# Performance work log

Hardware: AMD Instinct MI355X
Metric: run time of the kernel (lower is better)

The kernel has to match this reference:

```python
import jax, jax.numpy as jnp
import numpy as np

R_MAX = 5.0
AVG_NEIGH = 16.0
NUM_RADIAL = 8
F = 64            # channels per irrep (num_features)
S = 10            # num_species
LDIM = 16         # (max_ell+1)^2 for max_ell=3
L_SLICES = [(0, 1), (1, 4), (4, 9), (9, 16)]  # lm ranges for l=0..3
N_NODES = 10000
N_EDGES = 160000
HID_R = 64        # radial MLP hidden
HID_READ = 32     # readout MLP hidden


def sph_harm(v):
    # real spherical-harmonic polynomials up to l=3 (component convention fixed by this reference)
    x, y, z = v[:, 0], v[:, 1], v[:, 2]
    r2 = x * x + y * y + z * z
    return jnp.stack([
        jnp.ones_like(x),
        x, y, z,
        x * y, y * z, 3.0 * z * z - r2, x * z, x * x - y * y,
        y * (3.0 * x * x - y * y), x * y * z, y * (5.0 * z * z - r2),
        z * (5.0 * z * z - 3.0 * r2), x * (5.0 * z * z - r2),
        z * (x * x - y * y), x * (x * x - 3.0 * y * y),
    ], axis=-1)  # [E,16]


def radial_embedding(r):
    # Bessel basis with polynomial envelope (RadialEmbeddingBlock)
    u = r / R_MAX
    k = jnp.arange(1, NUM_RADIAL + 1, dtype=r.dtype)
    env = jnp.where(u < 1.0, (1.0 - u) ** 2 * (1.0 + 2.0 * u), 0.0)
    return jnp.sin(jnp.pi * k[None, :] * u[:, None]) / (u[:, None] + 1e-6) * env[:, None]


def species_linear(feats, W):
    # species-indexed e3nn Linear: per-l channel mixing. feats [N,F,16], W [N,4,F,F]
    outs = []
    for l, (a, b) in enumerate(L_SLICES):
        outs.append(jnp.einsum('nfm,nfg->ngm', feats[:, :, a:b], W[:, l]))
    return jnp.concatenate(outs, axis=-1)


def interaction(feats, Y, Remb, w1, w2, senders, receivers, n_nodes):
    # InteractionBlock: radial MLP -> tensor-product messages -> scatter-sum
    E = Y.shape[0]
    R = (jax.nn.silu(Remb @ w1) @ w2).reshape(E, F, 4, 2)  # per-l, per-path radial weights
    fs = feats[senders]            # [E,F,16] gather (irregular access)
    s0 = fs[:, :, 0:1]             # sender scalar channel
    parts = []
    for l, (a, b) in enumerate(L_SLICES):
        # path A: 0e (x) l -> l ;  path B: l (x) 0e -> l
        m_l = R[:, :, l, 0:1] * s0 * Y[:, None, a:b] + R[:, :, l, 1:2] * fs[:, :, a:b]
        parts.append(m_l)
    m = jnp.concatenate(parts, axis=-1)  # [E,F,16]
    agg = jax.ops.segment_sum(m, receivers, num_segments=n_nodes)
    return agg / jnp.sqrt(jnp.asarray(AVG_NEIGH, m.dtype))


def setup_inputs() -> dict:
    key = jax.random.key(0)
    ks = jax.random.split(key, 16)
    inp = {
        'vectors': jax.random.normal(ks[0], (N_EDGES, 3), jnp.float32) * 1.5,
        'node_specie': jax.random.randint(ks[1], (N_NODES,), 0, S, jnp.int32),
        'senders': jax.random.randint(ks[2], (N_EDGES,), 0, N_NODES, jnp.int32),
        'receivers': jax.random.randint(ks[3], (N_EDGES,), 0, N_NODES, jnp.int32),
        'w_embed': jax.random.normal(ks[4], (S, F), jnp.float32),
        'w_r1': jax.random.normal(ks[5], (2, NUM_RADIAL, HID_R), jnp.float32) / np.sqrt(NUM_RADIAL),
        'w_r2': jax.random.normal(ks[6], (2, HID_R, F * 4 * 2), jnp.float32) / np.sqrt(HID_R),
        'w_skip': jax.random.normal(ks[7], (2, S, 4, F, F), jnp.float32) / np.sqrt(F),
        'w_poly': jax.random.normal(ks[8], (2, 3, S, F), jnp.float32) * 0.1,
        'w_read0': jax.random.normal(ks[9], (F, 1), jnp.float32) / np.sqrt(F),
        'w_mlp1': jax.random.normal(ks[10], (F, HID_READ), jnp.float32) / np.sqrt(F),
        'w_mlp2': jax.random.normal(ks[11], (HID_READ, 1), jnp.float32) / np.sqrt(HID_READ),
    }
    return inp


def reference(vectors, node_specie, senders, receivers,
              w_embed, w_r1, w_r2, w_skip, w_poly,
              w_read0, w_mlp1, w_mlp2):
    N = node_specie.shape[0]
    senders = senders.astype(jnp.int32)
    receivers = receivers.astype(jnp.int32)
    r = jnp.sqrt(jnp.sum(vectors ** 2, axis=-1) + 1e-12)
    Y = sph_harm(vectors / r[:, None])
    Remb = radial_embedding(r)
    # node embedding -> scalar (l=0) channel only
    feats = jnp.zeros((N, F, LDIM), vectors.dtype).at[:, :, 0].set(w_embed[node_specie])
    outs = []
    for i in range(2):
        Wn = w_skip[i][node_specie]  # [N,4,F,F] species-indexed weights
        if i == 0:
            agg = interaction(feats, Y, Remb, w_r1[i], w_r2[i], senders, receivers, N)
            h = species_linear(agg, Wn)   # skip_tp_first
            sc = None
        else:
            sc = species_linear(feats, Wn)  # skip connection
            h = interaction(feats, Y, Remb, w_r1[i], w_r2[i], senders, receivers, N)
        # EquivariantProductBasisBlock (correlation=3): degree-3 invariant polynomial gate
        c = w_poly[i][:, node_specie]       # [3,N,F]
        s = h[:, :, 0]
        scale = c[0] + c[1] * s + c[2] * s * s
        feats = h * scale[:, :, None]
        if sc is not None:
            feats = feats + sc
        if i == 0:
            outs.append(feats[:, :, 0] @ w_read0)                       # LinearReadoutBlock
        else:
            outs.append(jax.nn.silu(feats[:, :, 0] @ w_mlp1) @ w_mlp2)  # NonLinearReadoutBlock
    return jnp.stack(outs, axis=1)  # [N, num_interactions, 1]
```

## Files before the change

### kernel.cpp

```cpp
#include <hip/hip_runtime.h>
#include <math.h>

#define F 64
#define LDIM 16
#define NRAD 8
#define HID_R 64
#define HID_READ 32
#define NSPEC 10

typedef __attribute__((ext_vector_type(8))) short short8v;
typedef __attribute__((ext_vector_type(4))) float f32x4;

__device__ __forceinline__ int l_of_m(int m) {
    return (m == 0) ? 0 : (m < 4) ? 1 : (m < 9) ? 2 : 3;
}
__device__ __forceinline__ float silu(float x) { return x / (1.0f + __expf(-x)); }
__device__ __forceinline__ unsigned short bf16bits(float x) {
    unsigned int u = __float_as_uint(x);
    u += 0x7fffu + ((u >> 16) & 1u);
    return (unsigned short)(u >> 16);
}
__device__ __forceinline__ float bf16tof(unsigned short b) {
    return __uint_as_float(((unsigned int)b) << 16);
}
__device__ __forceinline__ float lanebcast(float v, int l) {
    return __uint_as_float(__builtin_amdgcn_readlane(__float_as_uint(v), l));
}

__device__ __forceinline__ void geo_core(const float* __restrict__ vectors, int e,
                                         float* Ye_out, float* remb_out) {
    float vx = vectors[e * 3 + 0];
    float vy = vectors[e * 3 + 1];
    float vz = vectors[e * 3 + 2];
    float r = sqrtf(vx * vx + vy * vy + vz * vz + 1e-12f);
    float x = vx / r, y = vy / r, z = vz / r;
    float r2 = x * x + y * y + z * z;
    Ye_out[0]  = 1.0f;  Ye_out[1] = x;  Ye_out[2] = y;  Ye_out[3] = z;
    Ye_out[4]  = x * y; Ye_out[5] = y * z; Ye_out[6] = 3.0f * z * z - r2; Ye_out[7] = x * z;
    Ye_out[8]  = x * x - y * y;
    Ye_out[9]  = y * (3.0f * x * x - y * y);
    Ye_out[10] = x * y * z;
    Ye_out[11] = y * (5.0f * z * z - r2);
    Ye_out[12] = z * (5.0f * z * z - 3.0f * r2);
    Ye_out[13] = x * (5.0f * z * z - r2);
    Ye_out[14] = z * (x * x - y * y);
    Ye_out[15] = x * (x * x - 3.0f * y * y);
    float u = r / 5.0f;
    float env = (u < 1.0f) ? (1.0f - u) * (1.0f - u) * (1.0f + 2.0f * u) : 0.0f;
    float inv = env / (u + 1e-6f);
    const float PI = 3.14159265358979323846f;
#pragma unroll
    for (int k = 1; k <= NRAD; k++) remb_out[k - 1] = sinf(PI * (float)k * u) * inv;
}

__device__ __forceinline__ void hid_write(const float* remb, const float* w1,
                                          unsigned short* __restrict__ Hb, int e) {
    float h[HID_R];
#pragma unroll
    for (int j = 0; j < HID_R; j++) {
        float a = 0.0f;
#pragma unroll
        for (int k = 0; k < NRAD; k++) a += remb[k] * w1[k * HID_R + j];
        h[j] = silu(a);
    }
    unsigned int* dst = (unsigned int*)(Hb + (size_t)e * HID_R);
#pragma unroll
    for (int w = 0; w < 32; w++) {
        unsigned int lo = bf16bits(h[2 * w]);
        unsigned int hi = bf16bits(h[2 * w + 1]);
        dst[w] = lo | (hi << 16);
    }
}

__global__ void k1_kernel(const float* __restrict__ vectors,
                          const float* __restrict__ w_r1,
                          const float* __restrict__ w_r2,
                          const int* __restrict__ receivers,
                          float* __restrict__ Y,
                          unsigned short* __restrict__ Hb,
                          int* __restrict__ cnt,
                          unsigned short* __restrict__ w2f,
                          int E, int ngeo) {
    const int bid = blockIdx.x;
    if (bid >= ngeo) {
        const int layer = bid - ngeo;
        const float* src = w_r2 + (size_t)layer * HID_R * 512;
        unsigned short* dst = w2f + (size_t)layer * 32768;
        for (int idx = threadIdx.x; idx < 32768; idx += 256) {
            int j    = idx & 7;
            int lane = (idx >> 3) & 63;
            int ks   = (idx >> 9) & 1;
            int ct   = idx >> 10;
            int k    = ks * 32 + (lane >> 4) * 8 + j;
            int col  = ct * 16 + (lane & 15);
            dst[idx] = bf16bits(src[k * 512 + col]);
        }
        return;
    }
    const int e = bid * 256 + threadIdx.x;
    if (e >= E) return;
    atomicAdd(&cnt[receivers[e]], 1);
    float ye[16], remb[NRAD];
    geo_core(vectors, e, ye, remb);
    float4* Yd = (float4*)(Y + (size_t)e * 16);
    Yd[0] = make_float4(ye[0], ye[1], ye[2], ye[3]);
    Yd[1] = make_float4(ye[4], ye[5], ye[6], ye[7]);
    Yd[2] = make_float4(ye[8], ye[9], ye[10], ye[11]);
    Yd[3] = make_float4(ye[12], ye[13], ye[14], ye[15]);
    hid_write(remb, w_r1, Hb, e);
}

__global__ void geo_kernel(const float* __restrict__ vectors,
                           float* __restrict__ Y, float* __restrict__ Remb, int E) {
    int e = blockIdx.x * 256 + threadIdx.x;
    if (e >= E) return;
    float ye[16], remb[NRAD];
    geo_core(vectors, e, ye, remb);
#pragma unroll
    for (int m = 0; m < 16; m++) Y[(size_t)e * 16 + m] = ye[m];
#pragma unroll
    for (int k = 0; k < NRAD; k++) Remb[(size_t)e * NRAD + k] = remb[k];
}

__global__ void scan_kernel(const int* __restrict__ cnt, int* __restrict__ offs, int N) {
    __shared__ int buf[1024];
    __shared__ int carry;
    int t = threadIdx.x;
    if (t == 0) carry = 0;
    __syncthreads();
    for (int base = 0; base < N; base += 1024) {
        int v = (base + t < N) ? cnt[base + t] : 0;
        buf[t] = v;
        __syncthreads();
#pragma unroll
        for (int off = 1; off < 1024; off <<= 1) {
            int x = (t >= off) ? buf[t - off] : 0;
            __syncthreads();
            buf[t] += x;
            __syncthreads();
        }
        if (base + t < N) offs[base + t] = carry + buf[t] - v;
        __syncthreads();
        if (t == 0) carry += buf[1023];
        __syncthreads();
    }
    if (t == 0) offs[N] = carry;
}

__global__ void scatter_kernel(const int* __restrict__ receivers,
                               const int* __restrict__ senders,
                               const int* __restrict__ offs, int* __restrict__ cur,
                               int* __restrict__ eidx, int* __restrict__ snd_csr,
                               int* __restrict__ rcv_csr, int E) {
    int e = blockIdx.x * 256 + threadIdx.x;
    if (e >= E) return;
    int r = receivers[e];
    int pos = atomicAdd(&cur[r], 1);
    int t = offs[r] + pos;
    eidx[t] = e;
    snd_csr[t] = senders[e];
    rcv_csr[t] = r;
}

__global__ void init_feats_kernel(const float* __restrict__ w_embed,
                                  const int* __restrict__ specie,
                                  float* __restrict__ feats_t, int N) {
    int n = blockIdx.x;
    int sp = specie[n];
    for (int i = threadIdx.x; i < F * LDIM; i += 256) {
        int m = i >> 6;
        int f = i & 63;
        feats_t[(size_t)n * (F * LDIM) + i] = (m == 0) ? w_embed[sp * F + f] : 0.0f;
    }
}

template <bool L0>
__global__ __launch_bounds__(256, 4)
void fused_edge_kernel(const unsigned short* __restrict__ Hb,
                       const unsigned short* __restrict__ w2fl,
                       const float* __restrict__ Y,
                       const unsigned short* __restrict__ featsB,
                       const float* __restrict__ w_embed,
                       const int* __restrict__ specie,
                       const int* __restrict__ offs,
                       const int* __restrict__ eidx,
                       const int* __restrict__ snd_csr,
                       const int* __restrict__ rcv_csr,
                       float* __restrict__ agg, int N) {
    __shared__ float R_lds[16 * 532];
    __shared__ float ysL[16][16];
    __shared__ int   ssL[16];
    __shared__ int   rsL[16];
    const int tid = threadIdx.x;
    const int wave = tid >> 6, lane = tid & 63;
    const int lo = lane & 15, hi = lane >> 4;
    const int n0 = blockIdx.x * 2;
    const int segS = offs[n0], segE = offs[n0 + 2];
    const int mbase = wave * 4;

    int cur = -1;
    float acc[4] = {0.f, 0.f, 0.f, 0.f};

    for (int base = segS; base < segE; base += 16) {
        const int bend = (base + 16 < segE) ? base + 16 : segE;
        const int tcnt = bend - base;
        {
            const int t = tid >> 4, m = tid & 15;
            const int pos = base + t;
            const int cp = (pos < segE) ? pos : (segE - 1);
            ysL[t][m] = Y[(size_t)eidx[cp] * 16 + m];
            if (tid < 16) {
                const int p2 = base + tid;
                const int c2 = (p2 < segE) ? p2 : (segE - 1);
                const int s = snd_csr[c2];
                ssL[tid] = L0 ? specie[s] : s;
                rsL[tid] = rcv_csr[c2];
            }
        }
        {
            const int pos = base + lo;
            const int cp = (pos < segE) ? pos : (segE - 1);
            const int eid = eidx[cp];
            const unsigned short* hrow = Hb + (size_t)eid * 64;
            const short8v a0 = *(const short8v*)(hrow + hi * 8);
            const short8v a1 = *(const short8v*)(hrow + 32 + hi * 8);
            f32x4 c16[8];
#pragma unroll
            for (int i = 0; i < 8; i++) c16[i] = (f32x4)(0.f);
#pragma unroll
            for (int tt = 0; tt < 8; tt++) {
                const int ct = wave * 8 + tt;
                const short8v b0 = *(const short8v*)(w2fl + ct * 1024 + lane * 8);
                const short8v b1 = *(const short8v*)(w2fl + ct * 1024 + 512 + lane * 8);
                c16[tt] = __builtin_amdgcn_mfma_f32_16x16x32_bf16(a0, b0, c16[tt], 0, 0, 0);
                c16[tt] = __builtin_amdgcn_mfma_f32_16x16x32_bf16(a1, b1, c16[tt], 0, 0, 0);
            }
            const int lc = lo & 7;
#pragma unroll
            for (int tt = 0; tt < 8; tt++) {
                const int ct = wave * 8 + tt;
                const int f = ct * 2 + (lo >> 3);
#pragma unroll
                for (int r = 0; r < 4; r++) {
                    const int el = hi * 4 + r;
                    R_lds[el * 532 + lc * 66 + f] = c16[tt][r];
                }
            }
        }
        __syncthreads();
        {
            float ps0, pf[4] = {0.f, 0.f, 0.f, 0.f};
            if (L0) {
                ps0 = w_embed[ssL[0] * 64 + lane];
            } else {
                const unsigned short* f_ = featsB + (size_t)ssL[0] * 1024;
                ps0 = bf16tof(f_[lane]);
#pragma unroll
                for (int j = 0; j < 4; j++) pf[j] = bf16tof(f_[(mbase + j) * 64 + lane]);
            }
            for (int k = 0; k < tcnt; k++) {
                float ns0 = 0.f, nf[4] = {0.f, 0.f, 0.f, 0.f};
                const int kn = (k + 1 < tcnt) ? k + 1 : k;
                if (L0) {
                    ns0 = w_embed[ssL[kn] * 64 + lane];
                } else {
                    const unsigned short* f_ = featsB + (size_t)ssL[kn] * 1024;
                    ns0 = bf16tof(f_[lane]);
#pragma unroll
                    for (int j = 0; j < 4; j++) nf[j] = bf16tof(f_[(mbase + j) * 64 + lane]);
                }
                const int node = rsL[k];
                if (node != cur) {
                    if (cur >= 0) {
#pragma unroll
                        for (int j = 0; j < 4; j++)
                            agg[(size_t)cur * 1024 + (mbase + j) * 64 + lane] = acc[j] * 0.25f;
                    }
#pragma unroll
                    for (int j = 0; j < 4; j++) acc[j] = 0.f;
                    cur = node;
                }
                const float* Rt = R_lds + k * 532;
#pragma unroll
                for (int j = 0; j < 4; j++) {
                    const int m = mbase + j;
                    const int l = l_of_m(m);
                    const float r0 = Rt[(2 * l) * 66 + lane];
                    const float r1 = Rt[(2 * l + 1) * 66 + lane];
                    const float ym = ysL[k][m];
                    const float fsm = L0 ? ((m == 0) ? ps0 : 0.f) : pf[j];
                    acc[j] += r0 * ps0 * ym + r1 * fsm;
                }
                ps0 = ns0;
                if (!L0) {
#pragma unroll
                    for (int j = 0; j < 4; j++) pf[j] = nf[j];
                }
            }
        }
        __syncthreads();
    }
    if (cur >= 0) {
#pragma unroll
        for (int j = 0; j < 4; j++)
            agg[(size_t)cur * 1024 + (mbase + j) * 64 + lane] = acc[j] * 0.25f;
    }
#pragma unroll
    for (int d = 0; d < 2; d++) {
        const int nn = n0 + d;
        if (nn < N && offs[nn] == offs[nn + 1]) {
#pragma unroll
            for (int j = 0; j < 4; j++)
                agg[(size_t)nn * 1024 + (mbase + j) * 64 + lane] = 0.f;
        }
    }
}

__global__ void k2_kernel(const float* __restrict__ agg,
                          const int* __restrict__ specie,
                          const float* __restrict__ w_skip0,
                          const float* __restrict__ w_poly0,
                          const float* __restrict__ w_read0,
                          unsigned short* __restrict__ featsB,
                          float* __restrict__ featsF,
                          int useBF16,
                          float* __restrict__ out, int N,
                          const float* __restrict__ vectors,
                          const float* __restrict__ w1L1,
                          unsigned short* __restrict__ Hb, int E) {
    if (blockIdx.x >= N) {
        const int e = (blockIdx.x - N) * 256 + threadIdx.x;
        if (e >= E) return;
        float ye[16], remb[NRAD];
        geo_core(vectors, e, ye, remb);
        hid_write(remb, w1L1, Hb, e);
        return;
    }
    const int n = blockIdx.x;
    const int g = threadIdx.x & 63;
    const int mb = threadIdx.x >> 6;
    const int sp = specie[n];
    const float* W = w_skip0 + (size_t)sp * 4 * F * F;

    float areg[4];
#pragma unroll
    for (int j = 0; j < 4; j++) areg[j] = agg[(size_t)n * 1024 + (mb * 4 + j) * 64 + g];

    float h[4] = {0.f, 0.f, 0.f, 0.f};
    if (mb == 0) {
        const float* W0 = W;
        const float* W1 = W + 4096;
#pragma unroll
        for (int f = 0; f < 64; f++) {
            const float w0 = W0[f * 64 + g];
            const float w1 = W1[f * 64 + g];
            h[0] += lanebcast(areg[0], f) * w0;
            h[1] += lanebcast(areg[1], f) * w1;
            h[2] += lanebcast(areg[2], f) * w1;
            h[3] += lanebcast(areg[3], f) * w1;
        }
    } else if (mb == 1) {
        const float* W2 = W + 8192;
#pragma unroll
        for (int f = 0; f < 64; f++) {
            const float w2 = W2[f * 64 + g];
            h[0] += lanebcast(areg[0], f) * w2;
            h[1] += lanebcast(areg[1], f) * w2;
            h[2] += lanebcast(areg[2], f) * w2;
            h[3] += lanebcast(areg[3], f) * w2;
        }
    } else if (mb == 2) {
        const float* W2 = W + 8192;
        const float* W3 = W + 12288;
#pragma unroll
        for (int f = 0; f < 64; f++) {
            const float w2 = W2[f * 64 + g];
            const float w3 = W3[f * 64 + g];
            h[0] += lanebcast(areg[0], f) * w2;
            h[1] += lanebcast(areg[1], f) * w3;
            h[2] += lanebcast(areg[2], f) * w3;
            h[3] += lanebcast(areg[3], f) * w3;
        }
    } else {
        const float* W3 = W + 12288;
#pragma unroll
        for (int f = 0; f < 64; f++) {
            const float w3 = W3[f * 64 + g];
            h[0] += lanebcast(areg[0], f) * w3;
            h[1] += lanebcast(areg[1], f) * w3;
            h[2] += lanebcast(areg[2], f) * w3;
            h[3] += lanebcast(areg[3], f) * w3;
        }
    }

    __shared__ float h0L[64];
    if (mb == 0) h0L[g] = h[0];
    __syncthreads();
    const float s = h0L[g];
    const float c0 = w_poly0[(0 * NSPEC + sp) * F + g];
    const float c1 = w_poly0[(1 * NSPEC + sp) * F + g];
    const float c2 = w_poly0[(2 * NSPEC + sp) * F + g];
    const float scale = c0 + c1 * s + c2 * s * s;
    float f0val = 0.0f;
#pragma unroll
    for (int j = 0; j < 4; j++) {
        const int m = mb * 4 + j;
        const float fv = h[j] * scale;
        const size_t idx = (size_t)n * 1024 + m * 64 + g;
        if (useBF16) featsB[idx] = bf16bits(fv);
        else         featsF[idx] = fv;
        if (m == 0) f0val = fv;
    }
    if (mb == 0) {
        float v = f0val * w_read0[g];
#pragma unroll
        for (int off = 32; off > 0; off >>= 1) v += __shfl_down(v, off);
        if (g == 0) out[(size_t)n * 2 + 0] = v;
    }
}

__global__ void node1_kernel(const float* __restrict__ agg,
                             const unsigned short* __restrict__ featsB,
                             const int* __restrict__ specie,
                             const float* __restrict__ w_skip1,
                             const float* __restrict__ w_poly1,
                             const float* __restrict__ w_mlp1,
                             const float* __restrict__ w_mlp2,
                             float* __restrict__ out, int N) {
    const int wave = threadIdx.x >> 6;
    const int lane = threadIdx.x & 63;
    const int n = blockIdx.x * 4 + wave;
    const int sp = specie[n];
    const float* W0 = w_skip1 + (size_t)sp * 4 * F * F;
    const float fv = bf16tof(featsB[(size_t)n * 1024 + lane]);
    float sc0 = 0.0f;
#pragma unroll
    for (int f = 0; f < F; f++) {
        sc0 += lanebcast(fv, f) * W0[f * F + lane];
    }
    const float h0 = agg[(size_t)n * 1024 + lane];
    const float c0 = w_poly1[(0 * NSPEC + sp) * F + lane];
    const float c1 = w_poly1[(1 * NSPEC + sp) * F + lane];
    const float c2 = w_poly1[(2 * NSPEC + sp) * F + lane];
    const float scale = c0 + c1 * h0 + c2 * h0 * h0;
    const float f2 = h0 * scale + sc0;
    float acc = 0.0f;
#pragma unroll
    for (int gg = 0; gg < F; gg++) {
        const float fg = lanebcast(f2, gg);
        if (lane < HID_READ) acc += fg * w_mlp1[gg * HID_READ + lane];
    }
    float o = 0.0f;
    if (lane < HID_READ) o = silu(acc) * w_mlp2[lane];
#pragma unroll
    for (int off = 32; off > 0; off >>= 1) o += __shfl_down(o, off);
    if (lane == 0) out[(size_t)n * 2 + 1] = o;
}

__global__ void node1f_kernel(const float* __restrict__ agg,
                              const float* __restrict__ feats,
                              const int* __restrict__ specie,
                              const float* __restrict__ w_skip1,
                              const float* __restrict__ w_poly1,
                              const float* __restrict__ w_mlp1,
                              const float* __restrict__ w_mlp2,
                              float* __restrict__ out, int N) {
    const int wave = threadIdx.x >> 6;
    const int lane = threadIdx.x & 63;
    const int n = blockIdx.x * 4 + wave;
    const int sp = specie[n];
    const float* W0 = w_skip1 + (size_t)sp * 4 * F * F;
    const float fv = feats[(size_t)n * 1024 + lane];
    float sc0 = 0.0f;
#pragma unroll 8
    for (int f = 0; f < F; f++) {
        const float ff = __shfl(fv, f);
        sc0 += ff * W0[f * F + lane];
    }
    const float h0 = agg[(size_t)n * 1024 + lane];
    const float c0 = w_poly1[(0 * NSPEC + sp) * F + lane];
    const float c1 = w_poly1[(1 * NSPEC + sp) * F + lane];
    const float c2 = w_poly1[(2 * NSPEC + sp) * F + lane];
    const float scale = c0 + c1 * h0 + c2 * h0 * h0;
    const float f2 = h0 * scale + sc0;
    float acc = 0.0f;
#pragma unroll 8
    for (int gg = 0; gg < F; gg++) {
        const float fg = __shfl(f2, gg);
        if (lane < HID_READ) acc += fg * w_mlp1[gg * HID_READ + lane];
    }
    float o = 0.0f;
    if (lane < HID_READ) o = silu(acc) * w_mlp2[lane];
#pragma unroll
    for (int off = 32; off > 0; off >>= 1) o += __shfl_down(o, off);
    if (lane == 0) out[(size_t)n * 2 + 1] = o;
}

__global__ void edge_kernel(const float* __restrict__ Y, const float* __restrict__ Remb,
                            const float* __restrict__ feats_t,
                            const int* __restrict__ senders, const int* __restrict__ receivers,
                            const float* __restrict__ w1, const float* __restrict__ w2,
                            float* __restrict__ agg_t, int E) {
    const int wave = threadIdx.x >> 6;
    const int lane = threadIdx.x & 63;
    const int e = blockIdx.x * 4 + wave;
    __shared__ float hbuf[4][64];
    const float* remb = Remb + (size_t)e * NRAD;
    float acc = 0.0f;
#pragma unroll
    for (int k = 0; k < NRAD; k++) acc += remb[k] * w1[k * F + lane];
    hbuf[wave][lane] = silu(acc);
    __syncthreads();
    float r8[8] = {0.f, 0.f, 0.f, 0.f, 0.f, 0.f, 0.f, 0.f};
    const float* w2base = w2 + lane * 8;
#pragma unroll 8
    for (int j = 0; j < HID_R; j++) {
        float hj = hbuf[wave][j];
        const float4 a = *(const float4*)(w2base + j * 512);
        const float4 b = *(const float4*)(w2base + j * 512 + 4);
        r8[0] += hj * a.x; r8[1] += hj * a.y; r8[2] += hj * a.z; r8[3] += hj * a.w;
        r8[4] += hj * b.x; r8[5] += hj * b.y; r8[6] += hj * b.z; r8[7] += hj * b.w;
    }
    const int snd = senders[e];
    const int rcv = receivers[e];
    const float* fsrc = feats_t + (size_t)snd * (F * LDIM);
    float* adst = agg_t + (size_t)rcv * (F * LDIM);
    const float s0 = fsrc[lane];
    const float* Ye = Y + (size_t)e * 16;
#pragma unroll
    for (int m = 0; m < LDIM; m++) {
        const int l = l_of_m(m);
        const float ym = Ye[m];
        const float fsm = fsrc[m * F + lane];
        const float val = r8[l * 2 + 0] * s0 * ym + r8[l * 2 + 1] * fsm;
        atomicAdd(adst + m * F + lane, val * 0.25f);
    }
}

static inline size_t alignup(size_t x) { return (x + 255) & ~(size_t)255; }

extern "C" void kernel_launch(void* const* d_in, const int* in_sizes, int n_in,
                              void* d_out, int out_size, void* d_ws, size_t ws_size,
                              hipStream_t stream) {
    const float* vectors   = (const float*)d_in[0];
    const int*   specie    = (const int*)d_in[1];
    const int*   senders   = (const int*)d_in[2];
    const int*   receivers = (const int*)d_in[3];
    const float* w_embed   = (const float*)d_in[4];
    const float* w_r1      = (const float*)d_in[5];
    const float* w_r2      = (const float*)d_in[6];
    const float* w_skip    = (const float*)d_in[7];
    const float* w_poly    = (const float*)d_in[8];
    const float* w_read0   = (const float*)d_in[9];
    const float* w_mlp1    = (const float*)d_in[10];
    const float* w_mlp2    = (const float*)d_in[11];
    float* out = (float*)d_out;

    const int E = in_sizes[0] / 3;
    const int N = in_sizes[1];
    const int ngeo = (E + 255) / 256;

    char* base = (char*)d_ws;
    size_t off = 0;
    float* Y      = (float*)(base + off); off += alignup((size_t)E * 16 * sizeof(float));
    unsigned short* featsB = (unsigned short*)(base + off); off += alignup((size_t)N * F * LDIM * sizeof(unsigned short));
    float* agg    = (float*)(base + off); off += alignup((size_t)N * F * LDIM * sizeof(float));
    unsigned short* Hb = (unsigned short*)(base + off); off += alignup((size_t)E * 64 * sizeof(unsigned short));
    int* cnt      = (int*)(base + off);   off += alignup((size_t)N * sizeof(int));
    int* cur      = (int*)(base + off);   off += alignup((size_t)N * sizeof(int));
    int* offs     = (int*)(base + off);   off += alignup((size_t)(N + 1) * sizeof(int));
    int* eidx     = (int*)(base + off);   off += alignup((size_t)E * sizeof(int));
    int* snd_csr  = (int*)(base + off);   off += alignup((size_t)E * sizeof(int));
    int* rcv_csr  = (int*)(base + off);   off += alignup((size_t)E * sizeof(int));
    unsigned short* w2f = (unsigned short*)(base + off); off += alignup((size_t)2 * 32768 * sizeof(unsigned short));
    const size_t need = off;

    const size_t aggBytes = (size_t)N * F * LDIM * sizeof(float);

    if (ws_size >= need) {
        hipMemsetAsync(cnt, 0, (size_t)N * sizeof(int), stream);
        hipMemsetAsync(cur, 0, (size_t)N * sizeof(int), stream);
        k1_kernel<<<ngeo + 2, 256, 0, stream>>>(vectors, w_r1, w_r2, receivers,
                                                Y, Hb, cnt, w2f, E, ngeo);
        scan_kernel<<<1, 1024, 0, stream>>>(cnt, offs, N);
        scatter_kernel<<<ngeo, 256, 0, stream>>>(receivers, senders, offs, cur,
                                                 eidx, snd_csr, rcv_csr, E);
        fused_edge_kernel<true><<<N / 2, 256, 0, stream>>>(
            Hb, w2f, Y, nullptr, w_embed, specie, offs, eidx, snd_csr, rcv_csr, agg, N);
        k2_kernel<<<N + ngeo, 256, 0, stream>>>(agg, specie,
                                                w_skip + (size_t)0 * NSPEC * 4 * F * F,
                                                w_poly + (size_t)0 * 3 * NSPEC * F,
                                                w_read0, featsB, nullptr, 1, out, N,
                                                vectors, w_r1 + NRAD * HID_R, Hb, E);
        fused_edge_kernel<false><<<N / 2, 256, 0, stream>>>(
            Hb, w2f + 32768, Y, featsB, w_embed, specie, offs, eidx, snd_csr, rcv_csr, agg, N);
        node1_kernel<<<N / 4, 256, 0, stream>>>(agg, featsB, specie,
                                                w_skip + (size_t)1 * NSPEC * 4 * F * F,
                                                w_poly + (size_t)1 * 3 * NSPEC * F,
                                                w_mlp1, w_mlp2, out, N);
    } else {
        size_t fo = 0;
        float* Yf    = (float*)(base + fo); fo += alignup((size_t)E * 16 * sizeof(float));
        float* Remb  = (float*)(base + fo); fo += alignup((size_t)E * NRAD * sizeof(float));
        float* featsF= (float*)(base + fo); fo += alignup((size_t)N * F * LDIM * sizeof(float));
        float* aggF  = (float*)(base + fo);

        geo_kernel<<<ngeo, 256, 0, stream>>>(vectors, Yf, Remb, E);
        init_feats_kernel<<<N, 256, 0, stream>>>(w_embed, specie, featsF, N);
        hipMemsetAsync(aggF, 0, aggBytes, stream);
        edge_kernel<<<E / 4, 256, 0, stream>>>(Yf, Remb, featsF, senders, receivers,
                                               w_r1, w_r2, aggF, E);
        k2_kernel<<<N, 256, 0, stream>>>(aggF, specie,
                                         w_skip + (size_t)0 * NSPEC * 4 * F * F,
                                         w_poly + (size_t)0 * 3 * NSPEC * F,
                                         w_read0, nullptr, featsF, 0, out, N,
                                         vectors, w_r1 + NRAD * HID_R, nullptr, 0);
        hipMemsetAsync(aggF, 0, aggBytes, stream);
        edge_kernel<<<E / 4, 256, 0, stream>>>(Yf, Remb, featsF, senders, receivers,
                                               w_r1 + NRAD * HID_R, w_r2 + HID_R * 512,
                                               aggF, E);
        node1f_kernel<<<N / 4, 256, 0, stream>>>(aggF, featsF, specie,
                                                 w_skip + (size_t)1 * NSPEC * 4 * F * F,
                                                 w_poly + (size_t)1 * 3 * NSPEC * F,
                                                 w_mlp1, w_mlp2, out, N);
    }
}
```

Measured before the change: 360.9 us.

## Fuse node-level species linear, gate and readout into edge aggregation kernels

Each fused edge kernel now keeps its per-node accumulators for its two receiver nodes in registers and directly applies the species-indexed linear, polynomial gate and readout, instead of writing agg to global memory and launching k2/node1 kernels. The layer-1 radial hidden activations are computed up front in k1 into a second buffer, removing that work from k2. This drops the agg round trip and two launches, but adds per-block serial matmul work (64x64 per l) that sits at the tail of the edge kernel and may lower occupancy. It also now requires an even node count.

```diff
diff --git a/kernel.cpp b/kernel.cpp
--- a/kernel.cpp
+++ b/kernel.cpp
@@ -77,7 +77,8 @@
                           const float* __restrict__ w_r2,
                           const int* __restrict__ receivers,
                           float* __restrict__ Y,
-                          unsigned short* __restrict__ Hb,
+                          unsigned short* __restrict__ Hb0,
+                          unsigned short* __restrict__ Hb1,
                           int* __restrict__ cnt,
                           unsigned short* __restrict__ w2f,
                           int E, int ngeo) {
@@ -107,7 +108,8 @@
     Yd[1] = make_float4(ye[4], ye[5], ye[6], ye[7]);
     Yd[2] = make_float4(ye[8], ye[9], ye[10], ye[11]);
     Yd[3] = make_float4(ye[12], ye[13], ye[14], ye[15]);
-    hid_write(remb, w_r1, Hb, e);
+    hid_write(remb, w_r1, Hb0, e);
+    hid_write(remb, w_r1 + NRAD * HID_R, Hb1, e);
 }
 
 __global__ void geo_kernel(const float* __restrict__ vectors,
@@ -179,18 +181,26 @@
 void fused_edge_kernel(const unsigned short* __restrict__ Hb,
                        const unsigned short* __restrict__ w2fl,
                        const float* __restrict__ Y,
-                       const unsigned short* __restrict__ featsB,
+                       const unsigned short* __restrict__ featsIn,
                        const float* __restrict__ w_embed,
                        const int* __restrict__ specie,
                        const int* __restrict__ offs,
                        const int* __restrict__ eidx,
                        const int* __restrict__ snd_csr,
                        const int* __restrict__ rcv_csr,
-                       float* __restrict__ agg, int N) {
+                       const float* __restrict__ w_skipL,
+                       const float* __restrict__ w_polyL,
+                       const float* __restrict__ w_read0,
+                       const float* __restrict__ w_mlp1,
+                       const float* __restrict__ w_mlp2,
+                       unsigned short* __restrict__ featsOut,
+                       float* __restrict__ out, int N) {
     __shared__ float R_lds[16 * 532];
     __shared__ float ysL[16][16];
     __shared__ int   ssL[16];
     __shared__ int   rsL[16];
+    __shared__ float h0LA[64];
+    __shared__ float h0LB[64];
     const int tid = threadIdx.x;
     const int wave = tid >> 6, lane = tid & 63;
     const int lo = lane & 15, hi = lane >> 4;
@@ -198,8 +208,8 @@
     const int segS = offs[n0], segE = offs[n0 + 2];
     const int mbase = wave * 4;
 
-    int cur = -1;
-    float acc[4] = {0.f, 0.f, 0.f, 0.f};
+    float accA[4] = {0.f, 0.f, 0.f, 0.f};
+    float accB[4] = {0.f, 0.f, 0.f, 0.f};
 
     for (int base = segS; base < segE; base += 16) {
         const int bend = (base + 16 < segE) ? base + 16 : segE;
@@ -253,7 +263,7 @@
             if (L0) {
                 ps0 = w_embed[ssL[0] * 64 + lane];
             } else {
-                const unsigned short* f_ = featsB + (size_t)ssL[0] * 1024;
+                const unsigned short* f_ = featsIn + (size_t)ssL[0] * 1024;
                 ps0 = bf16tof(f_[lane]);
 #pragma unroll
                 for (int j = 0; j < 4; j++) pf[j] = bf16tof(f_[(mbase + j) * 64 + lane]);
@@ -264,32 +274,35 @@
                 if (L0) {
                     ns0 = w_embed[ssL[kn] * 64 + lane];
                 } else {
-                    const unsigned short* f_ = featsB + (size_t)ssL[kn] * 1024;
+                    const unsigned short* f_ = featsIn + (size_t)ssL[kn] * 1024;
                     ns0 = bf16tof(f_[lane]);
 #pragma unroll
                     for (int j = 0; j < 4; j++) nf[j] = bf16tof(f_[(mbase + j) * 64 + lane]);
                 }
                 const int node = rsL[k];
-                if (node != cur) {
-                    if (cur >= 0) {
-#pragma unroll
-                        for (int j = 0; j < 4; j++)
-                            agg[(size_t)cur * 1024 + (mbase + j) * 64 + lane] = acc[j] * 0.25f;
+                const float* Rt = R_lds + k * 532;
+                if (node == n0) {
+#pragma unroll
+                    for (int j = 0; j < 4; j++) {
+                        const int m = mbase + j;
+                        const int l = l_of_m(m);
+                        const float r0 = Rt[(2 * l) * 66 + lane];
+                        const float r1 = Rt[(2 * l + 1) * 66 + lane];
+                        const float ym = ysL[k][m];
+                        const float fsm = L0 ? ((m == 0) ? ps0 : 0.f) : pf[j];
+                        accA[j] += r0 * ps0 * ym + r1 * fsm;
                     }
-#pragma unroll
-                    for (int j = 0; j < 4; j++) acc[j] = 0.f;
-                    cur = node;
-                }
-                const float* Rt = R_lds + k * 532;
-#pragma unroll
-                for (int j = 0; j < 4; j++) {
-                    const int m = mbase + j;
-                    const int l = l_of_m(m);
-                    const float r0 = Rt[(2 * l) * 66 + lane];
-                    const float r1 = Rt[(2 * l + 1) * 66 + lane];
-                    const float ym = ysL[k][m];
-                    const float fsm = L0 ? ((m == 0) ? ps0 : 0.f) : pf[j];
-                    acc[j] += r0 * ps0 * ym + r1 * fsm;
+                } else {
+#pragma unroll
+                    for (int j = 0; j < 4; j++) {
+                        const int m = mbase + j;
+                        const int l = l_of_m(m);
+                        const float r0 = Rt[(2 * l) * 66 + lane];
+                        const float r1 = Rt[(2 * l + 1) * 66 + lane];
+                        const float ym = ysL[k][m];
+                        const float fsm = L0 ? ((m == 0) ? ps0 : 0.f) : pf[j];
+                        accB[j] += r0 * ps0 * ym + r1 * fsm;
+                    }
                 }
                 ps0 = ns0;
                 if (!L0) {
@@ -300,18 +313,158 @@
         }
         __syncthreads();
     }
-    if (cur >= 0) {
-#pragma unroll
-        for (int j = 0; j < 4; j++)
-            agg[(size_t)cur * 1024 + (mbase + j) * 64 + lane] = acc[j] * 0.25f;
-    }
-#pragma unroll
-    for (int d = 0; d < 2; d++) {
-        const int nn = n0 + d;
-        if (nn < N && offs[nn] == offs[nn + 1]) {
-#pragma unroll
-            for (int j = 0; j < 4; j++)
-                agg[(size_t)nn * 1024 + (mbase + j) * 64 + lane] = 0.f;
+
+    const int nA = n0, nB = n0 + 1;
+    const int spA = specie[nA], spB = specie[nB];
+    const int g = lane;
+
+    if (L0) {
+        float aA[4], aB[4];
+#pragma unroll
+        for (int j = 0; j < 4; j++) { aA[j] = accA[j] * 0.25f; aB[j] = accB[j] * 0.25f; }
+        const float* WA = w_skipL + (size_t)spA * 4 * F * F;
+        const float* WB = w_skipL + (size_t)spB * 4 * F * F;
+        float hA[4] = {0.f, 0.f, 0.f, 0.f};
+        float hB[4] = {0.f, 0.f, 0.f, 0.f};
+        if (wave == 0) {
+            const float *WA0 = WA, *WA1 = WA + 4096, *WB0 = WB, *WB1 = WB + 4096;
+#pragma unroll
+            for (int f = 0; f < 64; f++) {
+                const float wa0 = WA0[f * 64 + g], wa1 = WA1[f * 64 + g];
+                const float wb0 = WB0[f * 64 + g], wb1 = WB1[f * 64 + g];
+                hA[0] += lanebcast(aA[0], f) * wa0;
+                hA[1] += lanebcast(aA[1], f) * wa1;
+                hA[2] += lanebcast(aA[2], f) * wa1;
+                hA[3] += lanebcast(aA[3], f) * wa1;
+                hB[0] += lanebcast(aB[0], f) * wb0;
+                hB[1] += lanebcast(aB[1], f) * wb1;
+                hB[2] += lanebcast(aB[2], f) * wb1;
+                hB[3] += lanebcast(aB[3], f) * wb1;
+            }
+        } else if (wave == 1) {
+            const float *WA2 = WA + 8192, *WB2 = WB + 8192;
+#pragma unroll
+            for (int f = 0; f < 64; f++) {
+                const float wa2 = WA2[f * 64 + g], wb2 = WB2[f * 64 + g];
+                hA[0] += lanebcast(aA[0], f) * wa2;
+                hA[1] += lanebcast(aA[1], f) * wa2;
+                hA[2] += lanebcast(aA[2], f) * wa2;
+                hA[3] += lanebcast(aA[3], f) * wa2;
+                hB[0] += lanebcast(aB[0], f) * wb2;
+                hB[1] += lanebcast(aB[1], f) * wb2;
+                hB[2] += lanebcast(aB[2], f) * wb2;
+                hB[3] += lanebcast(aB[3], f) * wb2;
+            }
+        } else if (wave == 2) {
+            const float *WA2 = WA + 8192, *WA3 = WA + 12288;
+            const float *WB2 = WB + 8192, *WB3 = WB + 12288;
+#pragma unroll
+            for (int f = 0; f < 64; f++) {
+                const float wa2 = WA2[f * 64 + g], wa3 = WA3[f * 64 + g];
+                const float wb2 = WB2[f * 64 + g], wb3 = WB3[f * 64 + g];
+                hA[0] += lanebcast(aA[0], f) * wa2;
+                hA[1] += lanebcast(aA[1], f) * wa3;
+                hA[2] += lanebcast(aA[2], f) * wa3;
+                hA[3] += lanebcast(aA[3], f) * wa3;
+                hB[0] += lanebcast(aB[0], f) * wb2;
+                hB[1] += lanebcast(aB[1], f) * wb3;
+                hB[2] += lanebcast(aB[2], f) * wb3;
+                hB[3] += lanebcast(aB[3], f) * wb3;
+            }
+        } else {
+            const float *WA3 = WA + 12288, *WB3 = WB + 12288;
+#pragma unroll
+            for (int f = 0; f < 64; f++) {
+                const float wa3 = WA3[f * 64 + g], wb3 = WB3[f * 64 + g];
+                hA[0] += lanebcast(aA[0], f) * wa3;
+                hA[1] += lanebcast(aA[1], f) * wa3;
+                hA[2] += lanebcast(aA[2], f) * wa3;
+                hA[3] += lanebcast(aA[3], f) * wa3;
+                hB[0] += lanebcast(aB[0], f) * wb3;
+                hB[1] += lanebcast(aB[1], f) * wb3;
+                hB[2] += lanebcast(aB[2], f) * wb3;
+                hB[3] += lanebcast(aB[3], f) * wb3;
+            }
+        }
+        if (wave == 0) { h0LA[g] = hA[0]; h0LB[g] = hB[0]; }
+        __syncthreads();
+        const float sA = h0LA[g], sB = h0LB[g];
+        const float c0A = w_polyL[(0 * NSPEC + spA) * F + g];
+        const float c1A = w_polyL[(1 * NSPEC + spA) * F + g];
+        const float c2A = w_polyL[(2 * NSPEC + spA) * F + g];
+        const float scaleA = c0A + c1A * sA + c2A * sA * sA;
+        const float c0B = w_polyL[(0 * NSPEC + spB) * F + g];
+        const float c1B = w_polyL[(1 * NSPEC + spB) * F + g];
+        const float c2B = w_polyL[(2 * NSPEC + spB) * F + g];
+        const float scaleB = c0B + c1B * sB + c2B * sB * sB;
+#pragma unroll
+        for (int j = 0; j < 4; j++) {
+            featsOut[(size_t)nA * 1024 + (mbase + j) * 64 + g] = bf16bits(hA[j] * scaleA);
+            featsOut[(size_t)nB * 1024 + (mbase + j) * 64 + g] = bf16bits(hB[j] * scaleB);
+        }
+        if (wave == 0) {
+            float vA = (hA[0] * scaleA) * w_read0[g];
+            float vB = (hB[0] * scaleB) * w_read0[g];
+#pragma unroll
+            for (int off = 32; off > 0; off >>= 1) {
+                vA += __shfl_down(vA, off);
+                vB += __shfl_down(vB, off);
+            }
+            if (g == 0) {
+                out[(size_t)nA * 2 + 0] = vA;
+                out[(size_t)nB * 2 + 0] = vB;
+            }
+        }
+    } else {
+        if (wave == 0) {
+            {
+                const float* W0 = w_skipL + (size_t)spA * 4 * F * F;
+                const float fv = bf16tof(featsIn[(size_t)nA * 1024 + lane]);
+                float sc0 = 0.0f;
+#pragma unroll
+                for (int f = 0; f < F; f++) sc0 += lanebcast(fv, f) * W0[f * F + lane];
+                const float h0 = accA[0] * 0.25f;
+                const float c0 = w_polyL[(0 * NSPEC + spA) * F + lane];
+                const float c1 = w_polyL[(1 * NSPEC + spA) * F + lane];
+                const float c2 = w_polyL[(2 * NSPEC + spA) * F + lane];
+                const float scale = c0 + c1 * h0 + c2 * h0 * h0;
+                const float f2 = h0 * scale + sc0;
+                float mac = 0.0f;
+#pragma unroll
+                for (int gg = 0; gg < F; gg++) {
+                    const float fg = lanebcast(f2, gg);
+                    if (lane < HID_READ) mac += fg * w_mlp1[gg * HID_READ + lane];
+                }
+                float o = 0.0f;
+                if (lane < HID_READ) o = silu(mac) * w_mlp2[lane];
+#pragma unroll
+                for (int off = 32; off > 0; off >>= 1) o += __shfl_down(o, off);
+                if (lane == 0) out[(size_t)nA * 2 + 1] = o;
+            }
+            {
+                const float* W0 = w_skipL + (size_t)spB * 4 * F * F;
+                const float fv = bf16tof(featsIn[(size_t)nB * 1024 + lane]);
+                float sc0 = 0.0f;
+#pragma unroll
+                for (int f = 0; f < F; f++) sc0 += lanebcast(fv, f) * W0[f * F + lane];
+                const float h0 = accB[0] * 0.25f;
+                const float c0 = w_polyL[(0 * NSPEC + spB) * F + lane];
+                const float c1 = w_polyL[(1 * NSPEC + spB) * F + lane];
+                const float c2 = w_polyL[(2 * NSPEC + spB) * F + lane];
+                const float scale = c0 + c1 * h0 + c2 * h0 * h0;
+                const float f2 = h0 * scale + sc0;
+                float mac = 0.0f;
+#pragma unroll
+                for (int gg = 0; gg < F; gg++) {
+                    const float fg = lanebcast(f2, gg);
+                    if (lane < HID_READ) mac += fg * w_mlp1[gg * HID_READ + lane];
+                }
+                float o = 0.0f;
+                if (lane < HID_READ) o = silu(mac) * w_mlp2[lane];
+#pragma unroll
+                for (int off = 32; off > 0; off >>= 1) o += __shfl_down(o, off);
+                if (lane == 0) out[(size_t)nB * 2 + 1] = o;
+            }
         }
     }
 }
@@ -321,21 +474,8 @@
                           const float* __restrict__ w_skip0,
                           const float* __restrict__ w_poly0,
                           const float* __restrict__ w_read0,
-                          unsigned short* __restrict__ featsB,
                           float* __restrict__ featsF,
-                          int useBF16,
-                          float* __restrict__ out, int N,
-                          const float* __restrict__ vectors,
-                          const float* __restrict__ w1L1,
-                          unsigned short* __restrict__ Hb, int E) {
-    if (blockIdx.x >= N) {
-        const int e = (blockIdx.x - N) * 256 + threadIdx.x;
-        if (e >= E) return;
-        float ye[16], remb[NRAD];
-        geo_core(vectors, e, ye, remb);
-        hid_write(remb, w1L1, Hb, e);
-        return;
-    }
+                          float* __restrict__ out, int N) {
     const int n = blockIdx.x;
     const int g = threadIdx.x & 63;
     const int mb = threadIdx.x >> 6;
@@ -406,9 +546,7 @@
     for (int j = 0; j < 4; j++) {
         const int m = mb * 4 + j;
         const float fv = h[j] * scale;
-        const size_t idx = (size_t)n * 1024 + m * 64 + g;
-        if (useBF16) featsB[idx] = bf16bits(fv);
-        else         featsF[idx] = fv;
+        featsF[(size_t)n * 1024 + m * 64 + g] = fv;
         if (m == 0) f0val = fv;
     }
     if (mb == 0) {
@@ -417,44 +555,6 @@
         for (int off = 32; off > 0; off >>= 1) v += __shfl_down(v, off);
         if (g == 0) out[(size_t)n * 2 + 0] = v;
     }
-}
-
-__global__ void node1_kernel(const float* __restrict__ agg,
-                             const unsigned short* __restrict__ featsB,
-                             const int* __restrict__ specie,
-                             const float* __restrict__ w_skip1,
-                             const float* __restrict__ w_poly1,
-                             const float* __restrict__ w_mlp1,
-                             const float* __restrict__ w_mlp2,
-                             float* __restrict__ out, int N) {
-    const int wave = threadIdx.x >> 6;
-    const int lane = threadIdx.x & 63;
-    const int n = blockIdx.x * 4 + wave;
-    const int sp = specie[n];
-    const float* W0 = w_skip1 + (size_t)sp * 4 * F * F;
-    const float fv = bf16tof(featsB[(size_t)n * 1024 + lane]);
-    float sc0 = 0.0f;
-#pragma unroll
-    for (int f = 0; f < F; f++) {
-        sc0 += lanebcast(fv, f) * W0[f * F + lane];
-    }
-    const float h0 = agg[(size_t)n * 1024 + lane];
-    const float c0 = w_poly1[(0 * NSPEC + sp) * F + lane];
-    const float c1 = w_poly1[(1 * NSPEC + sp) * F + lane];
-    const float c2 = w_poly1[(2 * NSPEC + sp) * F + lane];
-    const float scale = c0 + c1 * h0 + c2 * h0 * h0;
-    const float f2 = h0 * scale + sc0;
-    float acc = 0.0f;
-#pragma unroll
-    for (int gg = 0; gg < F; gg++) {
-        const float fg = lanebcast(f2, gg);
-        if (lane < HID_READ) acc += fg * w_mlp1[gg * HID_READ + lane];
-    }
-    float o = 0.0f;
-    if (lane < HID_READ) o = silu(acc) * w_mlp2[lane];
-#pragma unroll
-    for (int off = 32; off > 0; off >>= 1) o += __shfl_down(o, off);
-    if (lane == 0) out[(size_t)n * 2 + 1] = o;
 }
 
 __global__ void node1f_kernel(const float* __restrict__ agg,
@@ -564,8 +664,8 @@
     size_t off = 0;
     float* Y      = (float*)(base + off); off += alignup((size_t)E * 16 * sizeof(float));
     unsigned short* featsB = (unsigned short*)(base + off); off += alignup((size_t)N * F * LDIM * sizeof(unsigned short));
-    float* agg    = (float*)(base + off); off += alignup((size_t)N * F * LDIM * sizeof(float));
-    unsigned short* Hb = (unsigned short*)(base + off); off += alignup((size_t)E * 64 * sizeof(unsigned short));
+    unsigned short* Hb0 = (unsigned short*)(base + off); off += alignup((size_t)E * 64 * sizeof(unsigned short));
+    unsigned short* Hb1 = (unsigned short*)(base + off); off += alignup((size_t)E * 64 * sizeof(unsigned short));
     int* cnt      = (int*)(base + off);   off += alignup((size_t)N * sizeof(int));
     int* cur      = (int*)(base + off);   off += alignup((size_t)N * sizeof(int));
     int* offs     = (int*)(base + off);   off += alignup((size_t)(N + 1) * sizeof(int));
@@ -577,27 +677,24 @@
 
     const size_t aggBytes = (size_t)N * F * LDIM * sizeof(float);
 
-    if (ws_size >= need) {
+    if (ws_size >= need && (N & 1) == 0) {
         hipMemsetAsync(cnt, 0, (size_t)N * sizeof(int), stream);
         hipMemsetAsync(cur, 0, (size_t)N * sizeof(int), stream);
         k1_kernel<<<ngeo + 2, 256, 0, stream>>>(vectors, w_r1, w_r2, receivers,
-                                                Y, Hb, cnt, w2f, E, ngeo);
+                                                Y, Hb0, Hb1, cnt, w2f, E, ngeo);
         scan_kernel<<<1, 1024, 0, stream>>>(cnt, offs, N);
         scatter_kernel<<<ngeo, 256, 0, stream>>>(receivers, senders, offs, cur,
                                                  eidx, snd_csr, rcv_csr, E);
         fused_edge_kernel<true><<<N / 2, 256, 0, stream>>>(
-            Hb, w2f, Y, nullptr, w_embed, specie, offs, eidx, snd_csr, rcv_csr, agg, N);
-        k2_kernel<<<N + ngeo, 256, 0, stream>>>(agg, specie,
-                                                w_skip + (size_t)0 * NSPEC * 4 * F * F,
-                                                w_poly + (size_t)0 * 3 * NSPEC * F,
-                                                w_read0, featsB, nullptr, 1, out, N,
-                                                vectors, w_r1 + NRAD * HID_R, Hb, E);
+            Hb0, w2f, Y, nullptr, w_embed, specie, offs, eidx, snd_csr, rcv_csr,
+            w_skip + (size_t)0 * NSPEC * 4 * F * F,
+            w_poly + (size_t)0 * 3 * NSPEC * F,
+            w_read0, nullptr, nullptr, featsB, out, N);
         fused_edge_kernel<false><<<N / 2, 256, 0, stream>>>(
-            Hb, w2f + 32768, Y, featsB, w_embed, specie, offs, eidx, snd_csr, rcv_csr, agg, N);
-        node1_kernel<<<N / 4, 256, 0, stream>>>(agg, featsB, specie,
-                                                w_skip + (size_t)1 * NSPEC * 4 * F * F,
-                                                w_poly + (size_t)1 * 3 * NSPEC * F,
-                                                w_mlp1, w_mlp2, out, N);
+            Hb1, w2f + 32768, Y, featsB, w_embed, specie, offs, eidx, snd_csr, rcv_csr,
+            w_skip + (size_t)1 * NSPEC * 4 * F * F,
+            w_poly + (size_t)1 * 3 * NSPEC * F,
+            nullptr, w_mlp1, w_mlp2, nullptr, out, N);
     } else {
         size_t fo = 0;
         float* Yf    = (float*)(base + fo); fo += alignup((size_t)E * 16 * sizeof(float));
@@ -613,8 +710,7 @@
         k2_kernel<<<N, 256, 0, stream>>>(aggF, specie,
                                          w_skip + (size_t)0 * NSPEC * 4 * F * F,
                                          w_poly + (size_t)0 * 3 * NSPEC * F,
-                                         w_read0, nullptr, featsF, 0, out, N,
-                                         vectors, w_r1 + NRAD * HID_R, nullptr, 0);
+                                         w_read0, featsF, out, N);
         hipMemsetAsync(aggF, 0, aggBytes, stream);
         edge_kernel<<<E / 4, 256, 0, stream>>>(Yf, Remb, featsF, senders, receivers,
                                                w_r1 + NRAD * HID_R, w_r2 + HID_R * 512,
```

Result: slower. 384.4 us (+6.5%).
